# Kernel tuning notes

Hardware: AMD Instinct MI355X
Metric: run time of the kernel (lower is better)

## Reference

```python
import jax, jax.numpy as jnp
import numpy as np

N_NODES = 50000
N_EDGES = 800000
HID = 128


def setup_inputs() -> dict:
    key = jax.random.key(0)
    ks = jax.random.split(key, 10)
    s_msg = 1.0 / np.sqrt(2 * HID + 1)
    s_u1 = 1.0 / np.sqrt(2 * HID)
    s_u2 = 1.0 / np.sqrt(HID)
    return {
        "z": jax.random.normal(ks[0], (N_NODES, HID), dtype=jnp.float32),
        "edge_weight": jax.random.uniform(ks[1], (N_EDGES,), dtype=jnp.float32),
        "edge_src": jax.random.randint(ks[2], (N_EDGES,), 0, N_NODES),
        "edge_dst": jax.random.randint(ks[3], (N_EDGES,), 0, N_NODES),
        "Wm": jax.random.normal(ks[4], (2 * HID + 1, HID), dtype=jnp.float32) * s_msg,
        "bm": jax.random.normal(ks[5], (HID,), dtype=jnp.float32) * s_msg,
        "W1": jax.random.normal(ks[6], (2 * HID, HID), dtype=jnp.float32) * s_u1,
        "b1": jax.random.normal(ks[7], (HID,), dtype=jnp.float32) * s_u1,
        "W2": jax.random.normal(ks[8], (HID, HID), dtype=jnp.float32) * s_u2,
        "b2": jax.random.normal(ks[9], (HID,), dtype=jnp.float32) * s_u2,
    }


def reference(z, edge_weight, edge_src, edge_dst, Wm, bm, W1, b1, W2, b2):
    n, H = z.shape
    # message Linear on concat([z[u], z[v], w]) split to avoid materializing [E, 2H+1]
    Wd, Ws, ww = Wm[:H], Wm[H:2 * H], Wm[2 * H]  # [H,H], [H,H], [H]
    msgs = (z[edge_dst] @ Wd + z[edge_src] @ Ws
            + edge_weight[:, None] * ww[None, :] + bm)  # [E, H]
    # max-aggregate messages per destination node; zeros for isolated nodes
    agg = jax.ops.segment_max(msgs, edge_dst, num_segments=n)  # [n, H], -inf if empty
    deg = jax.ops.segment_sum(jnp.ones_like(edge_weight), edge_dst, num_segments=n)
    agg = jnp.where(deg[:, None] > 0, agg, jnp.zeros((), dtype=z.dtype))
    # update MLP on concat([z, agg]) split into two GEMMs
    W1a, W1b = W1[:H], W1[H:]
    hidden = jax.nn.relu(z @ W1a + agg @ W1b + b1)  # [n, H]
    return hidden @ W2 + b2  # [n, H]
```

## Files before the change

### kernel.cpp

```cpp
#include <hip/hip_runtime.h>
#include <hip/hip_bf16.h>

#define HID 128

typedef short bf16x8 __attribute__((ext_vector_type(8)));
typedef float f32x4  __attribute__((ext_vector_type(4)));
typedef unsigned short u16;
typedef unsigned long long u64;

__device__ __forceinline__ u16 f2bf(float f) {
    __hip_bfloat16 h = __float2bfloat16(f);
    return *reinterpret_cast<u16*>(&h);
}
__device__ __forceinline__ float bf2f(u16 x) {
    unsigned u = ((unsigned)x) << 16;
    return __uint_as_float(u);
}
__device__ __forceinline__ u64 pack_rec(int dst, int src, float w) {
    int wq = (int)fmaf(w, 32768.f, 0.5f);
    wq = wq > 32767 ? 32767 : wq;
    return ((u64)(unsigned)dst << 31) | ((unsigned)src << 15) | (unsigned)wq;
}


__global__ __launch_bounds__(256)
void prep_hist(const float* __restrict__ z, const float* __restrict__ Wm,
               const float* __restrict__ W1, const float* __restrict__ W2,
               const int* __restrict__ edst,
               u16* __restrict__ Ab, u16* __restrict__ Wt, int* __restrict__ bhist,
               int N, int Mp, int E, int bz, int bw, int nbk)
{
    __shared__ int lh[128];
    const int b = blockIdx.x;
    const int t = threadIdx.x;
    if (b < bz) {
        const int idx4 = (b * 256 + t) * 4;
        if (idx4 >= Mp * 128) return;
        const int row = idx4 >> 7, col = idx4 & 127;
        ushort4 u;
        if (row < N) {
            const float4 v = *(const float4*)&z[(size_t)row * 128 + col];
            u.x = f2bf(v.x); u.y = f2bf(v.y); u.z = f2bf(v.z); u.w = f2bf(v.w);
        } else { u.x = 0; u.y = 0; u.z = 0; u.w = 0; }
        *(ushort4*)&Ab[(size_t)row * 256 + col] = u;
    } else if (b < bz + bw) {
        const int idx = (b - bz) * 256 + t;
        if (idx >= 81920) return;
        float v;
        if (idx < 32768) {
            const int nn = idx >> 7, k = idx & 127;
            v = (nn < 128) ? Wm[k * 128 + nn] : Wm[(128 + k) * 128 + (nn - 128)];
        } else if (idx < 65536) {
            const int j = idx - 32768, n = j >> 8, k = j & 255;
            v = W1[k * 128 + n];
        } else {
            const int j = idx - 65536, n = j >> 7, k = j & 127;
            v = W2[k * 128 + n];
        }
        Wt[idx] = f2bf(v);
    } else {
        if (t < 128) lh[t] = 0;
        __syncthreads();
        const int e0 = (b - bz - bw) * 4096;
        const int eend = min(e0 + 4096, E);
        for (int e = e0 + t; e < eend; e += 256)
            atomicAdd(&lh[edst[e] >> 9], 1);
        __syncthreads();
        if (t < nbk && lh[t] > 0) atomicAdd(&bhist[t], lh[t]);
    }
}

__global__ __launch_bounds__(256)
void bucket_scatter(const int* __restrict__ esrc, const int* __restrict__ edst,
                    const float* __restrict__ ew,
                    const int* __restrict__ bhist, int* __restrict__ brun,
                    u64* __restrict__ tmp, int E, int nbk)
{
    __shared__ int cnt[128];
    __shared__ int rbase[128];
    __shared__ int bbase[128];
    const int t = threadIdx.x;
    const int e0 = blockIdx.x * 4096;
    const int eend = min(e0 + 4096, E);

    if (t < 128) cnt[t] = 0;
    if (t == 0) {
        int run = 0;
        for (int i = 0; i < nbk; i++) { bbase[i] = run; run += bhist[i]; }
    }
    __syncthreads();

    if (eend - e0 == 4096) {
        int myb[16]; u64 myrec[16];
#pragma unroll
        for (int i = 0; i < 16; i++) {
            const int e = e0 + t + i * 256;
            const int d = edst[e];
            myb[i] = d >> 9;
            myrec[i] = pack_rec(d, esrc[e], ew[e]);
            atomicAdd(&cnt[myb[i]], 1);
        }
        __syncthreads();
        if (t < nbk && cnt[t] > 0) rbase[t] = bbase[t] + atomicAdd(&brun[t], cnt[t]);
        __syncthreads();
        if (t < 128) cnt[t] = 0;
        __syncthreads();
#pragma unroll
        for (int i = 0; i < 16; i++) {
            const int r = atomicAdd(&cnt[myb[i]], 1);
            tmp[(size_t)rbase[myb[i]] + r] = myrec[i];
        }
    } else {
        for (int e = e0 + t; e < eend; e += 256)
            atomicAdd(&cnt[edst[e] >> 9], 1);
        __syncthreads();
        if (t < nbk && cnt[t] > 0) rbase[t] = bbase[t] + atomicAdd(&brun[t], cnt[t]);
        __syncthreads();
        if (t < 128) cnt[t] = 0;
        __syncthreads();
        for (int e = e0 + t; e < eend; e += 256) {
            const int d = edst[e];
            const int bk = d >> 9;
            const int r = atomicAdd(&cnt[bk], 1);
            tmp[(size_t)rbase[bk] + r] = pack_rec(d, esrc[e], ew[e]);
        }
    }
}

__global__ __launch_bounds__(256)
void bucket_sort(const u64* __restrict__ tmp, const int* __restrict__ bhist,
                 int* __restrict__ offsets, unsigned* __restrict__ s_ew,
                 int N, int E, int nbk)
{
    __shared__ int cnt[512];
    __shared__ int cur[512];
    __shared__ int ps[256];
    __shared__ int sh_base[2];
    const int b = blockIdx.x;
    const int t = threadIdx.x;
    const int n0 = b << 9;
    const int nhi = min(512, N - n0);

    if (t == 0) {
        int run = 0;
        for (int i = 0; i < b; i++) run += bhist[i];
        sh_base[0] = run;
        sh_base[1] = run + bhist[b];
    }
    cnt[t] = 0; cnt[t + 256] = 0;
    __syncthreads();
    const int base = sh_base[0];
    const int endp = sh_base[1];

    for (int r = base + t; r < endp; r += 256)
        atomicAdd(&cnt[(int)(tmp[r] >> 31) - n0], 1);
    __syncthreads();

    const int a0 = cnt[2 * t], a1 = cnt[2 * t + 1];
    const int sp = a0 + a1;
    ps[t] = sp;
    __syncthreads();
    for (int off = 1; off < 256; off <<= 1) {
        int add = (t >= off) ? ps[t - off] : 0;
        __syncthreads();
        ps[t] += add;
        __syncthreads();
    }
    const int ex = ps[t] - sp;
    cur[2 * t]     = base + ex;
    cur[2 * t + 1] = base + ex + a0;
    __syncthreads();

    for (int i = t; i < nhi; i += 256) offsets[n0 + i] = cur[i];
    if (t == 0 && n0 + nhi == N) offsets[N] = E;

    for (int r = base + t; r < endp; r += 256) {
        const u64 rec = tmp[r];
        const int local = (int)(rec >> 31) - n0;
        const int pos = atomicAdd(&cur[local], 1);
        s_ew[pos] = (unsigned)(rec & 0x7FFFFFFFu);
    }
}

__global__ __launch_bounds__(256)
void gemm_P(const u16* __restrict__ Ab, const u16* __restrict__ Wds_t,
            u16* __restrict__ Pb, int Mp)
{
    __shared__ u16 As[64 * 136];
    const int row0 = blockIdx.x * 64;
    const int tid = threadIdx.x;
    const int wv = tid >> 6, lane = tid & 63;
    const int wy = wv & 1, wx = wv >> 1;
    const int q = lane >> 4, n = lane & 15;

#pragma unroll
    for (int i = 0; i < 4; i++) {
        const int chunk = i * 256 + tid;
        const int row = chunk >> 4;
        const int c8 = chunk & 15;
        *(bf16x8*)&As[row * 136 + c8 * 8] =
            *(const bf16x8*)&Ab[(size_t)(row0 + row) * 256 + c8 * 8];
    }
    __syncthreads();

    const u16* pAl = As + (wy * 32 + n) * 136 + q * 8;
    const u16* pB = Wds_t + (size_t)(wx * 128 + n) * 128 + q * 8;

    f32x4 acc[2][8];
#pragma unroll
    for (int i = 0; i < 2; i++)
#pragma unroll
        for (int j = 0; j < 8; j++) acc[i][j] = f32x4{0.f, 0.f, 0.f, 0.f};

#pragma unroll
    for (int kk = 0; kk < 128; kk += 32) {
        bf16x8 a0 = *(const bf16x8*)(pAl + kk);
        bf16x8 a1 = *(const bf16x8*)(pAl + 16 * 136 + kk);
        bf16x8 bfr[8];
#pragma unroll
        for (int ni = 0; ni < 8; ni++)
            bfr[ni] = *(const bf16x8*)(pB + (size_t)ni * 16 * 128 + kk);
#pragma unroll
        for (int ni = 0; ni < 8; ni++) {
            acc[0][ni] = __builtin_amdgcn_mfma_f32_16x16x32_bf16(a0, bfr[ni], acc[0][ni], 0, 0, 0);
            acc[1][ni] = __builtin_amdgcn_mfma_f32_16x16x32_bf16(a1, bfr[ni], acc[1][ni], 0, 0, 0);
        }
    }

#pragma unroll
    for (int mi = 0; mi < 2; mi++) {
#pragma unroll
        for (int ni = 0; ni < 8; ni++) {
            const int rbase = row0 + wy * 32 + mi * 16 + q * 4;
            const int c = wx * 128 + ni * 16 + n;
#pragma unroll
            for (int r = 0; r < 4; r++)
                Pb[(size_t)(rbase + r) * 256 + c] = f2bf(acc[mi][ni][r]);
        }
    }
}

__global__ __launch_bounds__(256)
void aggregate_kernel(const u16* __restrict__ Pb,
                      const float* __restrict__ bm,
                      const float* __restrict__ ww,
                      const int* __restrict__ offsets,
                      const unsigned* __restrict__ s_ew,
                      u16* __restrict__ Ab, int N, int Mp)
{
    const int t = threadIdx.x;
    const int lane = t & 63;
    const int nd = blockIdx.x * 4 + (t >> 6);
    if (nd >= Mp) return;
    const int h0 = lane * 2;
    u16* dst = &Ab[(size_t)nd * 256 + 128 + h0];
    if (nd >= N) { *(ushort2*)dst = make_ushort2(0, 0); return; }

    const int start = offsets[nd];
    const int end   = offsets[nd + 1];
    const float ww0 = ww[h0], ww1 = ww[h0 + 1];
    const float kq = 1.f / 32768.f;
    float m0 = -INFINITY, m1 = -INFINITY;

    int e = start;
    for (; e + 3 < end; e += 4) {
        const unsigned u0 = s_ew[e],     u1 = s_ew[e + 1];
        const unsigned u2 = s_ew[e + 2], u3 = s_ew[e + 3];
        const float w0 = (float)(u0 & 32767u) * kq;
        const float w1 = (float)(u1 & 32767u) * kq;
        const float w2 = (float)(u2 & 32767u) * kq;
        const float w3 = (float)(u3 & 32767u) * kq;
        const ushort2 z0 = *(const ushort2*)&Pb[(size_t)(u0 >> 15) * 256 + 128 + h0];
        const ushort2 z1 = *(const ushort2*)&Pb[(size_t)(u1 >> 15) * 256 + 128 + h0];
        const ushort2 z2 = *(const ushort2*)&Pb[(size_t)(u2 >> 15) * 256 + 128 + h0];
        const ushort2 z3 = *(const ushort2*)&Pb[(size_t)(u3 >> 15) * 256 + 128 + h0];
        const float a0 = fmaf(w0, ww0, bf2f(z0.x)), c0 = fmaf(w0, ww1, bf2f(z0.y));
        const float a1 = fmaf(w1, ww0, bf2f(z1.x)), c1 = fmaf(w1, ww1, bf2f(z1.y));
        const float a2 = fmaf(w2, ww0, bf2f(z2.x)), c2 = fmaf(w2, ww1, bf2f(z2.y));
        const float a3 = fmaf(w3, ww0, bf2f(z3.x)), c3 = fmaf(w3, ww1, bf2f(z3.y));
        m0 = fmaxf(m0, fmaxf(fmaxf(a0, a1), fmaxf(a2, a3)));
        m1 = fmaxf(m1, fmaxf(fmaxf(c0, c1), fmaxf(c2, c3)));
    }
    for (; e < end; e++) {
        const unsigned u0 = s_ew[e];
        const float w0 = (float)(u0 & 32767u) * kq;
        const ushort2 z0 = *(const ushort2*)&Pb[(size_t)(u0 >> 15) * 256 + 128 + h0];
        m0 = fmaxf(m0, fmaf(w0, ww0, bf2f(z0.x)));
        m1 = fmaxf(m1, fmaf(w0, ww1, bf2f(z0.y)));
    }

    ushort2 outv;
    if (end > start) {
        const ushort2 zd = *(const ushort2*)&Pb[(size_t)nd * 256 + h0];
        outv.x = f2bf(bf2f(zd.x) + bm[h0]     + m0);
        outv.y = f2bf(bf2f(zd.y) + bm[h0 + 1] + m1);
    } else { outv.x = 0; outv.y = 0; }
    *(ushort2*)dst = outv;
}

__global__ __launch_bounds__(256)
void gemm_HO(const u16* __restrict__ Ab, const u16* __restrict__ W1t,
             const float* __restrict__ b1, const u16* __restrict__ W2t,
             const float* __restrict__ b2, float* __restrict__ out, int Mstore)
{
    __shared__ u16 smem[64 * 264];

    const int row0 = blockIdx.x * 64;
    const int tid = threadIdx.x;
    const int wv = tid >> 6, lane = tid & 63;
    const int wy = wv & 1, wx = wv >> 1;
    const int q = lane >> 4, n = lane & 15;

#pragma unroll
    for (int i = 0; i < 8; i++) {
        const int chunk = i * 256 + tid;
        const int row = chunk >> 5;
        const int c8 = chunk & 31;
        *(bf16x8*)&smem[row * 264 + c8 * 8] =
            *(const bf16x8*)&Ab[(size_t)(row0 + row) * 256 + c8 * 8];
    }
    __syncthreads();

    f32x4 acc[2][4];

    {
        const u16* pAl = smem + (wy * 32 + n) * 264 + q * 8;
        const u16* pB = W1t + (size_t)(wx * 64 + n) * 256 + q * 8;

#pragma unroll
        for (int i = 0; i < 2; i++)
#pragma unroll
            for (int j = 0; j < 4; j++) acc[i][j] = f32x4{0.f, 0.f, 0.f, 0.f};

#pragma unroll
        for (int kk = 0; kk < 256; kk += 32) {
            bf16x8 b0 = *(const bf16x8*)(pB + kk);
            bf16x8 b1f = *(const bf16x8*)(pB + 16 * 256 + kk);
            bf16x8 b2f = *(const bf16x8*)(pB + 32 * 256 + kk);
            bf16x8 b3f = *(const bf16x8*)(pB + 48 * 256 + kk);
            bf16x8 a0 = *(const bf16x8*)(pAl + kk);
            bf16x8 a1 = *(const bf16x8*)(pAl + 16 * 264 + kk);
            acc[0][0] = __builtin_amdgcn_mfma_f32_16x16x32_bf16(a0, b0,  acc[0][0], 0, 0, 0);
            acc[0][1] = __builtin_amdgcn_mfma_f32_16x16x32_bf16(a0, b1f, acc[0][1], 0, 0, 0);
            acc[0][2] = __builtin_amdgcn_mfma_f32_16x16x32_bf16(a0, b2f, acc[0][2], 0, 0, 0);
            acc[0][3] = __builtin_amdgcn_mfma_f32_16x16x32_bf16(a0, b3f, acc[0][3], 0, 0, 0);
            acc[1][0] = __builtin_amdgcn_mfma_f32_16x16x32_bf16(a1, b0,  acc[1][0], 0, 0, 0);
            acc[1][1] = __builtin_amdgcn_mfma_f32_16x16x32_bf16(a1, b1f, acc[1][1], 0, 0, 0);
            acc[1][2] = __builtin_amdgcn_mfma_f32_16x16x32_bf16(a1, b2f, acc[1][2], 0, 0, 0);
            acc[1][3] = __builtin_amdgcn_mfma_f32_16x16x32_bf16(a1, b3f, acc[1][3], 0, 0, 0);
        }
    }
    __syncthreads();

#pragma unroll
    for (int mi = 0; mi < 2; mi++) {
#pragma unroll
        for (int ni = 0; ni < 4; ni++) {
            const int rl = wy * 32 + mi * 16 + q * 4;
            const int c = wx * 64 + ni * 16 + n;
#pragma unroll
            for (int r = 0; r < 4; r++) {
                float v = acc[mi][ni][r] + b1[c];
                smem[(rl + r) * 136 + c] = f2bf(fmaxf(v, 0.f));
            }
        }
    }
    __syncthreads();

    {
        const u16* pB = W2t + (size_t)(wx * 64 + n) * 128 + q * 8;
        const u16* pHl = smem + (wy * 32 + n) * 136 + q * 8;

#pragma unroll
        for (int i = 0; i < 2; i++)
#pragma unroll
            for (int j = 0; j < 4; j++) acc[i][j] = f32x4{0.f, 0.f, 0.f, 0.f};

#pragma unroll
        for (int kk = 0; kk < 128; kk += 32) {
            bf16x8 b0 = *(const bf16x8*)(pB + kk);
            bf16x8 b1f = *(const bf16x8*)(pB + 16 * 128 + kk);
            bf16x8 b2f = *(const bf16x8*)(pB + 32 * 128 + kk);
            bf16x8 b3f = *(const bf16x8*)(pB + 48 * 128 + kk);
            bf16x8 a0 = *(const bf16x8*)(pHl + kk);
            bf16x8 a1 = *(const bf16x8*)(pHl + 16 * 136 + kk);
            acc[0][0] = __builtin_amdgcn_mfma_f32_16x16x32_bf16(a0, b0,  acc[0][0], 0, 0, 0);
            acc[0][1] = __builtin_amdgcn_mfma_f32_16x16x32_bf16(a0, b1f, acc[0][1], 0, 0, 0);
            acc[0][2] = __builtin_amdgcn_mfma_f32_16x16x32_bf16(a0, b2f, acc[0][2], 0, 0, 0);
            acc[0][3] = __builtin_amdgcn_mfma_f32_16x16x32_bf16(a0, b3f, acc[0][3], 0, 0, 0);
            acc[1][0] = __builtin_amdgcn_mfma_f32_16x16x32_bf16(a1, b0,  acc[1][0], 0, 0, 0);
            acc[1][1] = __builtin_amdgcn_mfma_f32_16x16x32_bf16(a1, b1f, acc[1][1], 0, 0, 0);
            acc[1][2] = __builtin_amdgcn_mfma_f32_16x16x32_bf16(a1, b2f, acc[1][2], 0, 0, 0);
            acc[1][3] = __builtin_amdgcn_mfma_f32_16x16x32_bf16(a1, b3f, acc[1][3], 0, 0, 0);
        }

#pragma unroll
        for (int mi = 0; mi < 2; mi++) {
#pragma unroll
            for (int ni = 0; ni < 4; ni++) {
                const int rbase = row0 + wy * 32 + mi * 16 + q * 4;
                const int c = wx * 64 + ni * 16 + n;
#pragma unroll
                for (int r = 0; r < 4; r++) {
                    const int rr = rbase + r;
                    if (rr >= Mstore) continue;
                    out[(size_t)rr * 128 + c] = acc[mi][ni][r] + b2[c];
                }
            }
        }
    }
}

extern "C" void kernel_launch(void* const* d_in, const int* in_sizes, int n_in,
                              void* d_out, int out_size, void* d_ws, size_t ws_size,
                              hipStream_t stream) {
    const float* z    = (const float*)d_in[0];
    const float* ew   = (const float*)d_in[1];
    const int*   esrc = (const int*)d_in[2];
    const int*   edst = (const int*)d_in[3];
    const float* Wm   = (const float*)d_in[4];
    const float* bm   = (const float*)d_in[5];
    const float* W1   = (const float*)d_in[6];
    const float* b1   = (const float*)d_in[7];
    const float* W2   = (const float*)d_in[8];
    const float* b2   = (const float*)d_in[9];
    float* out = (float*)d_out;

    const int N  = in_sizes[0] / HID;
    const int E  = in_sizes[1];
    const int Mp = ((N + 63) / 64) * 64;
    const int nbk = (N + 511) / 512;

    char* w = (char*)d_ws;
    u16*  Ab      = (u16*)w;      w += (size_t)Mp * 256 * 2;
    u16*  Pb      = (u16*)w;      w += (size_t)Mp * 256 * 2;
    u16*  Wt      = (u16*)w;      w += (size_t)81920 * 2;
    int*  offsets = (int*)w;      w += (size_t)(N + 64) * 4;
    int*  bhist   = (int*)w;      w += 128 * 4;
    int*  brun    = (int*)w;      w += 128 * 4;
    unsigned* s_ew = (unsigned*)w; w += (size_t)E * 4;

    u64* tmp = (u64*)Pb;

    const int bz = (Mp * 32 + 255) / 256;
    const int bw = (81920 + 255) / 256;
    const int bh = (E + 4095) / 4096;

    hipMemsetAsync(bhist, 0, 256 * sizeof(int), stream);
    prep_hist<<<bz + bw + bh, 256, 0, stream>>>(z, Wm, W1, W2, edst, Ab, Wt, bhist,
                                                N, Mp, E, bz, bw, nbk);
    bucket_scatter<<<(E + 4095) / 4096, 256, 0, stream>>>(esrc, edst, ew, bhist, brun,
                                                          tmp, E, nbk);
    bucket_sort<<<nbk, 256, 0, stream>>>(tmp, bhist, offsets, s_ew, N, E, nbk);

    gemm_P<<<Mp / 64, 256, 0, stream>>>(Ab, Wt, Pb, Mp);
    aggregate_kernel<<<(Mp + 3) / 4, 256, 0, stream>>>(Pb, bm, Wm + 256 * 128,
                                                       offsets, s_ew, Ab, N, Mp);
    gemm_HO<<<Mp / 64, 256, 0, stream>>>(Ab, Wt + 32768, b1, Wt + 65536, b2, out, N);
}
```

Measured before the change: 232.2 us.

## Fuse edge scatter with message GEMM, halve sort bucket size, widen aggregation unroll

The edge bucket-scatter and the P = z·[Wd|Ws] GEMM now run as block ranges of one launch, so the tensor-core GEMM overlaps with the atomic-heavy scatter and one kernel launch is removed. The scatter temp buffer gets its own workspace region instead of aliasing Pb, which makes the fusion legal. Buckets shrink from 512 to 256 nodes, giving twice as many sort blocks for better parallelism, at the cost of more histogram entries. The aggregation loop is unrolled by 8 instead of 4 to keep more gathers in flight, which raises register pressure.

```diff
diff --git a/kernel.cpp b/kernel.cpp
--- a/kernel.cpp
+++ b/kernel.cpp
@@ -30,7 +30,7 @@
                u16* __restrict__ Ab, u16* __restrict__ Wt, int* __restrict__ bhist,
                int N, int Mp, int E, int bz, int bw, int nbk)
 {
-    __shared__ int lh[128];
+    __shared__ int lh[256];
     const int b = blockIdx.x;
     const int t = threadIdx.x;
     if (b < bz) {
@@ -59,70 +59,127 @@
         }
         Wt[idx] = f2bf(v);
     } else {
-        if (t < 128) lh[t] = 0;
+        lh[t] = 0;
         __syncthreads();
         const int e0 = (b - bz - bw) * 4096;
         const int eend = min(e0 + 4096, E);
         for (int e = e0 + t; e < eend; e += 256)
-            atomicAdd(&lh[edst[e] >> 9], 1);
+            atomicAdd(&lh[edst[e] >> 8], 1);
         __syncthreads();
         if (t < nbk && lh[t] > 0) atomicAdd(&bhist[t], lh[t]);
     }
 }
 
 __global__ __launch_bounds__(256)
-void bucket_scatter(const int* __restrict__ esrc, const int* __restrict__ edst,
-                    const float* __restrict__ ew,
-                    const int* __restrict__ bhist, int* __restrict__ brun,
-                    u64* __restrict__ tmp, int E, int nbk)
+void scatter_gemmP(const int* __restrict__ esrc, const int* __restrict__ edst,
+                   const float* __restrict__ ew,
+                   const int* __restrict__ bhist, int* __restrict__ brun,
+                   u64* __restrict__ tmp, int E, int nbk, int nsc,
+                   const u16* __restrict__ Ab, const u16* __restrict__ Wds_t,
+                   u16* __restrict__ Pb, int Mp)
 {
-    __shared__ int cnt[128];
-    __shared__ int rbase[128];
-    __shared__ int bbase[128];
+    __shared__ int cnt[256];
+    __shared__ int rbase[256];
+    __shared__ int bbase[256];
+    __shared__ u16 As[64 * 136];
     const int t = threadIdx.x;
-    const int e0 = blockIdx.x * 4096;
-    const int eend = min(e0 + 4096, E);
-
-    if (t < 128) cnt[t] = 0;
-    if (t == 0) {
-        int run = 0;
-        for (int i = 0; i < nbk; i++) { bbase[i] = run; run += bhist[i]; }
-    }
-    __syncthreads();
-
-    if (eend - e0 == 4096) {
-        int myb[16]; u64 myrec[16];
-#pragma unroll
-        for (int i = 0; i < 16; i++) {
-            const int e = e0 + t + i * 256;
-            const int d = edst[e];
-            myb[i] = d >> 9;
-            myrec[i] = pack_rec(d, esrc[e], ew[e]);
-            atomicAdd(&cnt[myb[i]], 1);
-        }
-        __syncthreads();
-        if (t < nbk && cnt[t] > 0) rbase[t] = bbase[t] + atomicAdd(&brun[t], cnt[t]);
-        __syncthreads();
-        if (t < 128) cnt[t] = 0;
-        __syncthreads();
-#pragma unroll
-        for (int i = 0; i < 16; i++) {
-            const int r = atomicAdd(&cnt[myb[i]], 1);
-            tmp[(size_t)rbase[myb[i]] + r] = myrec[i];
+
+    if (blockIdx.x < nsc) {
+        const int e0 = blockIdx.x * 4096;
+        const int eend = min(e0 + 4096, E);
+
+        cnt[t] = 0;
+        if (t == 0) {
+            int run = 0;
+            for (int i = 0; i < nbk; i++) { bbase[i] = run; run += bhist[i]; }
+        }
+        __syncthreads();
+
+        if (eend - e0 == 4096) {
+            int myb[16]; u64 myrec[16];
+#pragma unroll
+            for (int i = 0; i < 16; i++) {
+                const int e = e0 + t + i * 256;
+                const int d = edst[e];
+                myb[i] = d >> 8;
+                myrec[i] = pack_rec(d, esrc[e], ew[e]);
+                atomicAdd(&cnt[myb[i]], 1);
+            }
+            __syncthreads();
+            if (t < nbk && cnt[t] > 0) rbase[t] = bbase[t] + atomicAdd(&brun[t], cnt[t]);
+            __syncthreads();
+            cnt[t] = 0;
+            __syncthreads();
+#pragma unroll
+            for (int i = 0; i < 16; i++) {
+                const int r = atomicAdd(&cnt[myb[i]], 1);
+                tmp[(size_t)rbase[myb[i]] + r] = myrec[i];
+            }
+        } else {
+            for (int e = e0 + t; e < eend; e += 256)
+                atomicAdd(&cnt[edst[e] >> 8], 1);
+            __syncthreads();
+            if (t < nbk && cnt[t] > 0) rbase[t] = bbase[t] + atomicAdd(&brun[t], cnt[t]);
+            __syncthreads();
+            cnt[t] = 0;
+            __syncthreads();
+            for (int e = e0 + t; e < eend; e += 256) {
+                const int d = edst[e];
+                const int bk = d >> 8;
+                const int r = atomicAdd(&cnt[bk], 1);
+                tmp[(size_t)rbase[bk] + r] = pack_rec(d, esrc[e], ew[e]);
+            }
         }
     } else {
-        for (int e = e0 + t; e < eend; e += 256)
-            atomicAdd(&cnt[edst[e] >> 9], 1);
-        __syncthreads();
-        if (t < nbk && cnt[t] > 0) rbase[t] = bbase[t] + atomicAdd(&brun[t], cnt[t]);
-        __syncthreads();
-        if (t < 128) cnt[t] = 0;
-        __syncthreads();
-        for (int e = e0 + t; e < eend; e += 256) {
-            const int d = edst[e];
-            const int bk = d >> 9;
-            const int r = atomicAdd(&cnt[bk], 1);
-            tmp[(size_t)rbase[bk] + r] = pack_rec(d, esrc[e], ew[e]);
+        const int row0 = (blockIdx.x - nsc) * 64;
+        const int wv = t >> 6, lane = t & 63;
+        const int wy = wv & 1, wx = wv >> 1;
+        const int q = lane >> 4, n = lane & 15;
+
+#pragma unroll
+        for (int i = 0; i < 4; i++) {
+            const int chunk = i * 256 + t;
+            const int row = chunk >> 4;
+            const int c8 = chunk & 15;
+            *(bf16x8*)&As[row * 136 + c8 * 8] =
+                *(const bf16x8*)&Ab[(size_t)(row0 + row) * 256 + c8 * 8];
+        }
+        __syncthreads();
+
+        const u16* pAl = As + (wy * 32 + n) * 136 + q * 8;
+        const u16* pB = Wds_t + (size_t)(wx * 128 + n) * 128 + q * 8;
+
+        f32x4 acc[2][8];
+#pragma unroll
+        for (int i = 0; i < 2; i++)
+#pragma unroll
+            for (int j = 0; j < 8; j++) acc[i][j] = f32x4{0.f, 0.f, 0.f, 0.f};
+
+#pragma unroll
+        for (int kk = 0; kk < 128; kk += 32) {
+            bf16x8 a0 = *(const bf16x8*)(pAl + kk);
+            bf16x8 a1 = *(const bf16x8*)(pAl + 16 * 136 + kk);
+            bf16x8 bfr[8];
+#pragma unroll
+            for (int ni = 0; ni < 8; ni++)
+                bfr[ni] = *(const bf16x8*)(pB + (size_t)ni * 16 * 128 + kk);
+#pragma unroll
+            for (int ni = 0; ni < 8; ni++) {
+                acc[0][ni] = __builtin_amdgcn_mfma_f32_16x16x32_bf16(a0, bfr[ni], acc[0][ni], 0, 0, 0);
+                acc[1][ni] = __builtin_amdgcn_mfma_f32_16x16x32_bf16(a1, bfr[ni], acc[1][ni], 0, 0, 0);
+            }
+        }
+
+#pragma unroll
+        for (int mi = 0; mi < 2; mi++) {
+#pragma unroll
+            for (int ni = 0; ni < 8; ni++) {
+                const int rbase2 = row0 + wy * 32 + mi * 16 + q * 4;
+                const int c = wx * 128 + ni * 16 + n;
+#pragma unroll
+                for (int r = 0; r < 4; r++)
+                    Pb[(size_t)(rbase2 + r) * 256 + c] = f2bf(acc[mi][ni][r]);
+            }
         }
     }
 }
@@ -132,14 +189,14 @@
                  int* __restrict__ offsets, unsigned* __restrict__ s_ew,
                  int N, int E, int nbk)
 {
-    __shared__ int cnt[512];
-    __shared__ int cur[512];
+    __shared__ int cnt[256];
+    __shared__ int cur[256];
     __shared__ int ps[256];
     __shared__ int sh_base[2];
     const int b = blockIdx.x;
     const int t = threadIdx.x;
-    const int n0 = b << 9;
-    const int nhi = min(512, N - n0);
+    const int n0 = b << 8;
+    const int nhi = min(256, N - n0);
 
     if (t == 0) {
         int run = 0;
@@ -147,7 +204,7 @@
         sh_base[0] = run;
         sh_base[1] = run + bhist[b];
     }
-    cnt[t] = 0; cnt[t + 256] = 0;
+    cnt[t] = 0;
     __syncthreads();
     const int base = sh_base[0];
     const int endp = sh_base[1];
@@ -156,9 +213,8 @@
         atomicAdd(&cnt[(int)(tmp[r] >> 31) - n0], 1);
     __syncthreads();
 
-    const int a0 = cnt[2 * t], a1 = cnt[2 * t + 1];
-    const int sp = a0 + a1;
-    ps[t] = sp;
+    const int v = cnt[t];
+    ps[t] = v;
     __syncthreads();
     for (int off = 1; off < 256; off <<= 1) {
         int add = (t >= off) ? ps[t - off] : 0;
@@ -166,12 +222,10 @@
         ps[t] += add;
         __syncthreads();
     }
-    const int ex = ps[t] - sp;
-    cur[2 * t]     = base + ex;
-    cur[2 * t + 1] = base + ex + a0;
-    __syncthreads();
-
-    for (int i = t; i < nhi; i += 256) offsets[n0 + i] = cur[i];
+    cur[t] = base + ps[t] - v;
+    __syncthreads();
+
+    if (t < nhi) offsets[n0 + t] = cur[t];
     if (t == 0 && n0 + nhi == N) offsets[N] = E;
 
     for (int r = base + t; r < endp; r += 256) {
@@ -179,64 +233,6 @@
         const int local = (int)(rec >> 31) - n0;
         const int pos = atomicAdd(&cur[local], 1);
         s_ew[pos] = (unsigned)(rec & 0x7FFFFFFFu);
-    }
-}
-
-__global__ __launch_bounds__(256)
-void gemm_P(const u16* __restrict__ Ab, const u16* __restrict__ Wds_t,
-            u16* __restrict__ Pb, int Mp)
-{
-    __shared__ u16 As[64 * 136];
-    const int row0 = blockIdx.x * 64;
-    const int tid = threadIdx.x;
-    const int wv = tid >> 6, lane = tid & 63;
-    const int wy = wv & 1, wx = wv >> 1;
-    const int q = lane >> 4, n = lane & 15;
-
-#pragma unroll
-    for (int i = 0; i < 4; i++) {
-        const int chunk = i * 256 + tid;
-        const int row = chunk >> 4;
-        const int c8 = chunk & 15;
-        *(bf16x8*)&As[row * 136 + c8 * 8] =
-            *(const bf16x8*)&Ab[(size_t)(row0 + row) * 256 + c8 * 8];
-    }
-    __syncthreads();
-
-    const u16* pAl = As + (wy * 32 + n) * 136 + q * 8;
-    const u16* pB = Wds_t + (size_t)(wx * 128 + n) * 128 + q * 8;
-
-    f32x4 acc[2][8];
-#pragma unroll
-    for (int i = 0; i < 2; i++)
-#pragma unroll
-        for (int j = 0; j < 8; j++) acc[i][j] = f32x4{0.f, 0.f, 0.f, 0.f};
-
-#pragma unroll
-    for (int kk = 0; kk < 128; kk += 32) {
-        bf16x8 a0 = *(const bf16x8*)(pAl + kk);
-        bf16x8 a1 = *(const bf16x8*)(pAl + 16 * 136 + kk);
-        bf16x8 bfr[8];
-#pragma unroll
-        for (int ni = 0; ni < 8; ni++)
-            bfr[ni] = *(const bf16x8*)(pB + (size_t)ni * 16 * 128 + kk);
-#pragma unroll
-        for (int ni = 0; ni < 8; ni++) {
-            acc[0][ni] = __builtin_amdgcn_mfma_f32_16x16x32_bf16(a0, bfr[ni], acc[0][ni], 0, 0, 0);
-            acc[1][ni] = __builtin_amdgcn_mfma_f32_16x16x32_bf16(a1, bfr[ni], acc[1][ni], 0, 0, 0);
-        }
-    }
-
-#pragma unroll
-    for (int mi = 0; mi < 2; mi++) {
-#pragma unroll
-        for (int ni = 0; ni < 8; ni++) {
-            const int rbase = row0 + wy * 32 + mi * 16 + q * 4;
-            const int c = wx * 128 + ni * 16 + n;
-#pragma unroll
-            for (int r = 0; r < 4; r++)
-                Pb[(size_t)(rbase + r) * 256 + c] = f2bf(acc[mi][ni][r]);
-        }
     }
 }
 
@@ -263,23 +259,24 @@
     float m0 = -INFINITY, m1 = -INFINITY;
 
     int e = start;
-    for (; e + 3 < end; e += 4) {
-        const unsigned u0 = s_ew[e],     u1 = s_ew[e + 1];
-        const unsigned u2 = s_ew[e + 2], u3 = s_ew[e + 3];
-        const float w0 = (float)(u0 & 32767u) * kq;
-        const float w1 = (float)(u1 & 32767u) * kq;
-        const float w2 = (float)(u2 & 32767u) * kq;
-        const float w3 = (float)(u3 & 32767u) * kq;
-        const ushort2 z0 = *(const ushort2*)&Pb[(size_t)(u0 >> 15) * 256 + 128 + h0];
-        const ushort2 z1 = *(const ushort2*)&Pb[(size_t)(u1 >> 15) * 256 + 128 + h0];
-        const ushort2 z2 = *(const ushort2*)&Pb[(size_t)(u2 >> 15) * 256 + 128 + h0];
-        const ushort2 z3 = *(const ushort2*)&Pb[(size_t)(u3 >> 15) * 256 + 128 + h0];
-        const float a0 = fmaf(w0, ww0, bf2f(z0.x)), c0 = fmaf(w0, ww1, bf2f(z0.y));
-        const float a1 = fmaf(w1, ww0, bf2f(z1.x)), c1 = fmaf(w1, ww1, bf2f(z1.y));
-        const float a2 = fmaf(w2, ww0, bf2f(z2.x)), c2 = fmaf(w2, ww1, bf2f(z2.y));
-        const float a3 = fmaf(w3, ww0, bf2f(z3.x)), c3 = fmaf(w3, ww1, bf2f(z3.y));
-        m0 = fmaxf(m0, fmaxf(fmaxf(a0, a1), fmaxf(a2, a3)));
-        m1 = fmaxf(m1, fmaxf(fmaxf(c0, c1), fmaxf(c2, c3)));
+    for (; e + 7 < end; e += 8) {
+        unsigned u[8]; ushort2 zz[8];
+#pragma unroll
+        for (int i = 0; i < 8; i++) u[i] = s_ew[e + i];
+#pragma unroll
+        for (int i = 0; i < 8; i++)
+            zz[i] = *(const ushort2*)&Pb[(size_t)(u[i] >> 15) * 256 + 128 + h0];
+        float ma[8], mb[8];
+#pragma unroll
+        for (int i = 0; i < 8; i++) {
+            const float wq = (float)(u[i] & 32767u) * kq;
+            ma[i] = fmaf(wq, ww0, bf2f(zz[i].x));
+            mb[i] = fmaf(wq, ww1, bf2f(zz[i].y));
+        }
+        m0 = fmaxf(m0, fmaxf(fmaxf(fmaxf(ma[0], ma[1]), fmaxf(ma[2], ma[3])),
+                             fmaxf(fmaxf(ma[4], ma[5]), fmaxf(ma[6], ma[7]))));
+        m1 = fmaxf(m1, fmaxf(fmaxf(fmaxf(mb[0], mb[1]), fmaxf(mb[2], mb[3])),
+                             fmaxf(fmaxf(mb[4], mb[5]), fmaxf(mb[6], mb[7]))));
     }
     for (; e < end; e++) {
         const unsigned u0 = s_ew[e];
@@ -429,31 +426,30 @@
     const int N  = in_sizes[0] / HID;
     const int E  = in_sizes[1];
     const int Mp = ((N + 63) / 64) * 64;
-    const int nbk = (N + 511) / 512;
+    const int nbk = (N + 255) / 256;
 
     char* w = (char*)d_ws;
     u16*  Ab      = (u16*)w;      w += (size_t)Mp * 256 * 2;
     u16*  Pb      = (u16*)w;      w += (size_t)Mp * 256 * 2;
     u16*  Wt      = (u16*)w;      w += (size_t)81920 * 2;
     int*  offsets = (int*)w;      w += (size_t)(N + 64) * 4;
-    int*  bhist   = (int*)w;      w += 128 * 4;
-    int*  brun    = (int*)w;      w += 128 * 4;
+    int*  bhist   = (int*)w;      w += 256 * 4;
+    int*  brun    = (int*)w;      w += 256 * 4;
     unsigned* s_ew = (unsigned*)w; w += (size_t)E * 4;
-
-    u64* tmp = (u64*)Pb;
+    u64*  tmp     = (u64*)w;      w += (size_t)E * 8;
 
     const int bz = (Mp * 32 + 255) / 256;
     const int bw = (81920 + 255) / 256;
     const int bh = (E + 4095) / 4096;
-
-    hipMemsetAsync(bhist, 0, 256 * sizeof(int), stream);
+    const int nsc = (E + 4095) / 4096;
+
+    hipMemsetAsync(bhist, 0, 512 * sizeof(int), stream);
     prep_hist<<<bz + bw + bh, 256, 0, stream>>>(z, Wm, W1, W2, edst, Ab, Wt, bhist,
                                                 N, Mp, E, bz, bw, nbk);
-    bucket_scatter<<<(E + 4095) / 4096, 256, 0, stream>>>(esrc, edst, ew, bhist, brun,
-                                                          tmp, E, nbk);
+    scatter_gemmP<<<nsc + Mp / 64, 256, 0, stream>>>(esrc, edst, ew, bhist, brun,
+                                                     tmp, E, nbk, nsc,
+                                                     Ab, Wt, Pb, Mp);
     bucket_sort<<<nbk, 256, 0, stream>>>(tmp, bhist, offsets, s_ew, N, E, nbk);
-
-    gemm_P<<<Mp / 64, 256, 0, stream>>>(Ab, Wt, Pb, Mp);
     aggregate_kernel<<<(Mp + 3) / 4, 256, 0, stream>>>(Pb, bm, Wm + 256 * 128,
                                                        offsets, s_ew, Ab, N, Mp);
     gemm_HO<<<Mp / 64, 256, 0, stream>>>(Ab, Wt + 32768, b1, Wt + 65536, b2, out, N);
```

Measured after the change: 220.6 us. 5.0% less time.
